# Kernel optimization log

Hardware: AMD Instinct MI355X
Metric: run time of the kernel (lower is better)

## Reference

```python
import jax, jax.numpy as jnp
import numpy as np

B, L, DL, DM, K = 8192, 1, 1024, 1024, 8


def setup_inputs() -> dict:
    key = jax.random.key(0)
    ks = jax.random.split(key, 8)
    s = lambda k, shape, sc=1.0: jax.random.normal(k, shape, jnp.float32) * sc
    return {
        "l_hidden": s(ks[0], (B, L, DL)),
        "m_hidden": s(ks[1], (B, L, DM)),
        "G_l_m": s(ks[2], (DL, K, DM)),   # randn'd each fwd in torch; exposed as input
        "G_m_l": s(ks[3], (DM, K, DL)),
        "l_fc1_w": s(ks[4], (256, DL), 0.02),
        "l_fc1_b": jnp.zeros((256,), jnp.float32),
        "l_fc2_w": s(ks[5], (DL, 256), 0.02),
        "l_fc2_b": jnp.zeros((DL,), jnp.float32),
        "m_fc1_w": s(ks[6], (128, DM), 0.02),
        "m_fc1_b": jnp.zeros((128,), jnp.float32),
        "m_fc2_w": s(ks[7], (DM, 128), 0.02),
        "m_fc2_b": jnp.zeros((DM,), jnp.float32),
    }


def _cross(h_a, h_b, G, g_vec):
    """One direction of the cross-share unit.
    h_a: [B,L,Da], h_b: [B,L,Db], G: [Da,K,Db], g_vec: [B,L,Da]. L must be 1.
    Broadcasts G over batch instead of torch's .repeat (same math, no 256GB copy).
    """
    b, l, da = h_a.shape
    k = G.shape[1]
    # l_hidden @ reshape(G, [Da, K*Db]) -> reshape to [B, L*K, Db]
    s = jnp.einsum('bld,dke->blke', h_a, G).reshape(b, l * k, -1)      # [B,L*K,Db]
    # tanh( shared @ h_b^T ) -> [B, L*K, L]
    t = jnp.tanh(jnp.einsum('bke,bse->bks', s, h_b))                    # [B,L*K,L]
    # reshape [B,L,K,L] -> permute [B,L,L,K] -> [B,L*L,K]
    t = t.reshape(b, l, k, l).transpose(0, 1, 3, 2).reshape(b, l * l, k)
    g = jnp.tile(g_vec, (1, k, 1))                                      # [B,L*K,Da] (L=1 -> [B,K,Da])
    vec = jnp.matmul(t, g)                                              # [B,L*L,Da]
    attn = jax.nn.softmax(vec, axis=-1)
    out = h_a + attn * h_a
    return out, attn


def reference(l_hidden, m_hidden, G_l_m, G_m_l,
              l_fc1_w, l_fc1_b, l_fc2_w, l_fc2_b,
              m_fc1_w, m_fc1_b, m_fc2_w, m_fc2_b):
    # dropout(0.3) is identity in eval mode
    G_vec_l = (l_hidden @ l_fc1_w.T + l_fc1_b) @ l_fc2_w.T + l_fc2_b   # [B,L,DL]
    G_vec_m = (m_hidden @ m_fc1_w.T + m_fc1_b) @ m_fc2_w.T + m_fc2_b   # [B,L,DM]
    l_out, l_attn = _cross(l_hidden, m_hidden, G_l_m, G_vec_l)
    m_out, m_attn = _cross(m_hidden, l_hidden, G_m_l, G_vec_m)
    return l_out, m_out, l_attn, m_attn
```

## Files before the change

kernel.cpp:

```cpp
#include <hip/hip_runtime.h>


#define NB 8192
#define DD 1024

typedef __bf16 bf16x8 __attribute__((ext_vector_type(8)));
typedef float f32x4 __attribute__((ext_vector_type(4)));

__device__ __forceinline__ unsigned short f2bf(float f) {
  unsigned u = __float_as_uint(f);
  u += 0x7FFFu + ((u >> 16) & 1u);
  return (unsigned short)(u >> 16);
}
__device__ __forceinline__ float bf2f(unsigned short h) {
  return __uint_as_float(((unsigned)h) << 16);
}

__global__ __launch_bounds__(256) void split_cast_k(
    const float* __restrict__ in, unsigned short* __restrict__ hi,
    unsigned short* __restrict__ lo, int n4) {
  int i = blockIdx.x * 256 + threadIdx.x;
  if (i >= n4) return;
  float4 v = reinterpret_cast<const float4*>(in)[i];
  float vv[4] = {v.x, v.y, v.z, v.w};
  unsigned short hh[4], ll[4];
#pragma unroll
  for (int c = 0; c < 4; ++c) {
    hh[c] = f2bf(vv[c]);
    ll[c] = f2bf(vv[c] - bf2f(hh[c]));
  }
  reinterpret_cast<ushort4*>(hi)[i] = make_ushort4(hh[0], hh[1], hh[2], hh[3]);
  reinterpret_cast<ushort4*>(lo)[i] = make_ushort4(ll[0], ll[1], ll[2], ll[3]);
}

__global__ __launch_bounds__(256) void transpose_split_k(
    const float* __restrict__ G, unsigned short* __restrict__ bhi,
    unsigned short* __restrict__ blo) {
  __shared__ float t[32][33];
  int c0 = blockIdx.x * 32;
  int d0 = blockIdx.y * 32;
  int tx = threadIdx.x & 31;
  int tg = threadIdx.x >> 5;
#pragma unroll
  for (int s = 0; s < 4; ++s) {
    int dr = tg * 4 + s;
    t[dr][tx] = G[(size_t)(d0 + dr) * 8192 + c0 + tx];
  }
  __syncthreads();
#pragma unroll
  for (int s = 0; s < 4; ++s) {
    int cr = tg * 4 + s;
    float v = t[tx][cr];
    size_t o = (size_t)(c0 + cr) * 1024 + d0 + tx;
    unsigned short h = f2bf(v);
    bhi[o] = h;
    blo[o] = f2bf(v - bf2f(h));
  }
}

__global__ __launch_bounds__(256) void wct_k(
    const float* __restrict__ w1, const float* __restrict__ b1,
    const float* __restrict__ w2, const float* __restrict__ b2, int J,
    unsigned short* __restrict__ bhi, unsigned short* __restrict__ blo,
    float* __restrict__ bc) {
  __shared__ float w2row[256];
  int n = blockIdx.x;
  int tid = threadIdx.x;
  if (tid < J) w2row[tid] = w2[n * J + tid];
  __syncthreads();
#pragma unroll
  for (int s = 0; s < 4; ++s) {
    int i = tid + s * 256;
    float acc = 0.f;
    for (int j = 0; j < J; ++j) acc = fmaf(w2row[j], w1[j * 1024 + i], acc);
    size_t o = (size_t)(8192 + n) * 1024 + i;
    unsigned short h = f2bf(acc);
    bhi[o] = h;
    blo[o] = f2bf(acc - bf2f(h));
  }
  if (tid == 0) {
    float acc = 0.f;
    for (int j = 0; j < J; ++j) acc = fmaf(w2row[j], b1[j], acc);
    bc[n] = acc + b2[n];
  }
}

#define SBAR() do { asm volatile("" ::: "memory"); __builtin_amdgcn_s_barrier(); asm volatile("" ::: "memory"); } while (0)
#define WAITV0() asm volatile("s_waitcnt vmcnt(0)" ::: "memory")
#define WAITV2() asm volatile("s_waitcnt vmcnt(2)" ::: "memory")

#define GLOAD(SRC, DST)                                              \
  __builtin_amdgcn_global_load_lds(                                  \
      (const __attribute__((address_space(1))) void*)(SRC),          \
      (__attribute__((address_space(3))) void*)(lds + (DST)), 16, 0, 0)

__global__ __launch_bounds__(512, 2) void gemm_k(
    const unsigned short* __restrict__ Ahi_, const unsigned short* __restrict__ Alo_,
    const unsigned short* __restrict__ Bhi_, const unsigned short* __restrict__ Blo_,
    const float* __restrict__ hb, float* __restrict__ gvec, float* __restrict__ x) {
  __shared__ __align__(16) char lds[131072];
  const char* Ah = (const char*)Ahi_;
  const char* Al = (const char*)Alo_;
  const char* Bh = (const char*)Bhi_;
  const char* Bl = (const char*)Blo_;

  const int tid = threadIdx.x;
  const int lane = tid & 63;
  const int wid = tid >> 6;
  const int wm = wid >> 2, wn = wid & 3;

  const int bid = blockIdx.x;
  const int xcd = bid & 7;
  const int j = bid >> 3;
  const int by = xcd * 4 + (j & 3);
  const int bx = j >> 2;
  const int m0 = by * 256;
  const int n0 = bx * 256;
  const bool isg = (n0 >= 8192);
  const int nt = isg ? 16 : 48;

  const int rowl = tid >> 3;
  const int colsw = ((tid & 7) ^ ((tid >> 3) & 7)) << 4;
  const int s0 = ((lane >> 4) ^ (lane & 7)) << 4;
  const int s1 = s0 ^ 64;

  f32x4 acc[4][4][2] = {};

  auto stage = [&](int tl, int q) {
    if (tl >= nt) return;
    const int seg = tl >> 4;
    const char* mat;
    int rowbase, dst;
    if (q < 2) {
      mat = (seg == 1) ? Al : Ah;
      rowbase = m0 + q * 128;
      dst = (tl & 1) * 32768 + q * 16384;
    } else {
      mat = (seg == 2) ? Bl : Bh;
      rowbase = n0 + (q - 2) * 128;
      dst = 65536 + (tl & 1) * 32768 + (q - 2) * 16384;
    }
    const char* src = mat + (size_t)(rowbase + rowl) * 2048 + ((tl & 15) << 7) + colsw;
    dst += wid * 1024;
    GLOAD(src, dst);
    GLOAD(src + 64 * 2048, dst + 8192);
  };

  auto ldA = [&](bf16x8 (*d)[2], int qa, int cb) {
    const char* p = lds + cb + qa * 16384 + (wm * 64 + (lane & 15)) * 128;
#pragma unroll
    for (int f = 0; f < 4; ++f) {
      d[f][0] = *reinterpret_cast<const bf16x8*>(p + f * 2048 + s0);
      d[f][1] = *reinterpret_cast<const bf16x8*>(p + f * 2048 + s1);
    }
  };
  auto ldB = [&](bf16x8 (*d)[2], int qb, int cb) {
    const char* p = lds + 65536 + cb + qb * 16384 + (wn * 32 + (lane & 15)) * 128;
#pragma unroll
    for (int g = 0; g < 2; ++g) {
      d[g][0] = *reinterpret_cast<const bf16x8*>(p + g * 2048 + s0);
      d[g][1] = *reinterpret_cast<const bf16x8*>(p + g * 2048 + s1);
    }
  };
  auto mm = [&](f32x4 (*ac)[2], bf16x8 (*aa)[2], bf16x8 (*bb)[2]) {
#pragma unroll
    for (int f = 0; f < 4; ++f)
#pragma unroll
      for (int g = 0; g < 2; ++g) {
        ac[f][g] = __builtin_amdgcn_mfma_f32_16x16x32_bf16(aa[f][0], bb[g][0], ac[f][g], 0, 0, 0);
        ac[f][g] = __builtin_amdgcn_mfma_f32_16x16x32_bf16(aa[f][1], bb[g][1], ac[f][g], 0, 0, 0);
      }
  };

  stage(0, 0); stage(0, 2); stage(0, 3); stage(0, 1);
  WAITV2();
  SBAR();

  bf16x8 af[4][2], af2[4][2], bv[2][2], bv2[2][2];
  for (int t = 0; t < nt; ++t) {
    const int cb = (t & 1) * 32768;
    ldA(af, 0, cb);
    ldB(bv, 0, cb);
    ldB(bv2, 1, cb);
    stage(t + 1, 0);
    __builtin_amdgcn_s_setprio(1);
    mm(acc[0], af, bv);
    __builtin_amdgcn_s_setprio(0);
    if (t + 1 < nt) { WAITV2(); } else { WAITV0(); }
    SBAR();
    ldA(af2, 1, cb);
    stage(t + 1, 2);
    __builtin_amdgcn_s_setprio(1);
    mm(acc[1], af, bv2);
    __builtin_amdgcn_s_setprio(0);
    SBAR();
    stage(t + 1, 3);
    __builtin_amdgcn_s_setprio(1);
    mm(acc[2], af2, bv2);
    __builtin_amdgcn_s_setprio(0);
    SBAR();
    stage(t + 1, 1);
    __builtin_amdgcn_s_setprio(1);
    mm(acc[3], af2, bv);
    __builtin_amdgcn_s_setprio(0);
    WAITV2();
    SBAR();
  }

  const int coll = lane & 15;
  const int rg = (lane >> 4) * 4;
  if (isg) {
#pragma unroll
    for (int q = 0; q < 4; ++q) {
      const int qm = (q >= 2);
      const int qn = (q == 1 || q == 2);
#pragma unroll
      for (int f = 0; f < 4; ++f)
#pragma unroll
        for (int rr = 0; rr < 4; ++rr) {
          const int row = m0 + qm * 128 + wm * 64 + f * 16 + rg + rr;
#pragma unroll
          for (int g = 0; g < 2; ++g) {
            const int gcol = (n0 - 8192) + qn * 128 + wn * 32 + g * 16 + coll;
            gvec[(size_t)row * 1024 + gcol] = acc[q][f][g][rr];
          }
        }
    }
  } else {
    const int kidx = n0 >> 10;
    const int ebase = (n0 & 1023) + wn * 32 + coll;
#pragma unroll
    for (int qm = 0; qm < 2; ++qm) {
      f32x4 (*acA)[2] = acc[qm ? 3 : 0];
      f32x4 (*acB)[2] = acc[qm ? 2 : 1];
#pragma unroll
      for (int f = 0; f < 4; ++f)
#pragma unroll
        for (int rr = 0; rr < 4; ++rr) {
          const int row = m0 + qm * 128 + wm * 64 + f * 16 + rg + rr;
          const float* hr = hb + (size_t)row * 1024 + ebase;
          float tmp = acA[f][0][rr] * hr[0] + acA[f][1][rr] * hr[16] +
                      acB[f][0][rr] * hr[128] + acB[f][1][rr] * hr[144];
#pragma unroll
          for (int s = 1; s < 16; s <<= 1) tmp += __shfl_xor(tmp, s);
          if (coll == 0) atomicAdd(&x[row * 8 + kidx], tmp);
        }
    }
  }
}

__global__ __launch_bounds__(256) void finalize_k(
    const float* __restrict__ xk, const float* __restrict__ gvec,
    const float* __restrict__ bc, const float* __restrict__ ha,
    float* __restrict__ out, float* __restrict__ attn) {
  int b = blockIdx.x;
  int tid = threadIdx.x;
  float S = 0.f;
#pragma unroll
  for (int k = 0; k < 8; ++k) S += tanhf(xk[b * 8 + k]);
  float v[4];
  float mx = -3.4e38f;
#pragma unroll
  for (int s = 0; s < 4; ++s) {
    int d = tid + s * 256;
    v[s] = S * (gvec[(size_t)b * 1024 + d] + bc[d]);
    mx = fmaxf(mx, v[s]);
  }
  __shared__ float red[8];
#pragma unroll
  for (int off = 32; off >= 1; off >>= 1) mx = fmaxf(mx, __shfl_xor(mx, off));
  int lane = tid & 63, w = tid >> 6;
  if (lane == 0) red[w] = mx;
  __syncthreads();
  float m = fmaxf(fmaxf(red[0], red[1]), fmaxf(red[2], red[3]));
  float e[4], sum = 0.f;
#pragma unroll
  for (int s = 0; s < 4; ++s) { e[s] = __expf(v[s] - m); sum += e[s]; }
#pragma unroll
  for (int off = 32; off >= 1; off >>= 1) sum += __shfl_xor(sum, off);
  if (lane == 0) red[4 + w] = sum;
  __syncthreads();
  float inv = 1.f / (red[4] + red[5] + red[6] + red[7]);
#pragma unroll
  for (int s = 0; s < 4; ++s) {
    int d = tid + s * 256;
    float a = e[s] * inv;
    attn[(size_t)b * 1024 + d] = a;
    float h = ha[(size_t)b * 1024 + d];
    out[(size_t)b * 1024 + d] = fmaf(a, h, h);
  }
}

extern "C" void kernel_launch(void* const* d_in, const int* in_sizes, int n_in,
                              void* d_out, int out_size, void* d_ws, size_t ws_size,
                              hipStream_t stream) {
  const float* l_hidden = (const float*)d_in[0];
  const float* m_hidden = (const float*)d_in[1];
  const float* G_l_m = (const float*)d_in[2];
  const float* G_m_l = (const float*)d_in[3];
  const float* l_fc1_w = (const float*)d_in[4];
  const float* l_fc1_b = (const float*)d_in[5];
  const float* l_fc2_w = (const float*)d_in[6];
  const float* l_fc2_b = (const float*)d_in[7];
  const float* m_fc1_w = (const float*)d_in[8];
  const float* m_fc1_b = (const float*)d_in[9];
  const float* m_fc2_w = (const float*)d_in[10];
  const float* m_fc2_b = (const float*)d_in[11];
  float* out = (float*)d_out;

  char* ws = (char*)d_ws;
  unsigned short* Ahi = (unsigned short*)(ws);
  unsigned short* Alo = (unsigned short*)(ws + 16777216);
  unsigned short* Bhi = (unsigned short*)(ws + 33554432);
  unsigned short* Blo = (unsigned short*)(ws + 52428800);
  float* gvec = (float*)(ws + 71303168);
  float* x = (float*)(ws + 104857600);
  float* bc = (float*)(ws + 105381888);

  hipMemsetAsync(x, 0, 2 * NB * 8 * sizeof(float), stream);

  const size_t BD = (size_t)NB * DD;
  dim3 gemmGrid(1152);

  split_cast_k<<<(int)(BD / 4 / 256), 256, 0, stream>>>(l_hidden, Ahi, Alo, (int)(BD / 4));
  transpose_split_k<<<dim3(256, 32), 256, 0, stream>>>(G_l_m, Bhi, Blo);
  wct_k<<<1024, 256, 0, stream>>>(l_fc1_w, l_fc1_b, l_fc2_w, l_fc2_b, 256, Bhi, Blo, bc);
  gemm_k<<<gemmGrid, 512, 0, stream>>>(Ahi, Alo, Bhi, Blo, m_hidden, gvec, x);
  finalize_k<<<NB, 256, 0, stream>>>(x, gvec, bc, l_hidden, out, out + 2 * BD);

  split_cast_k<<<(int)(BD / 4 / 256), 256, 0, stream>>>(m_hidden, Ahi, Alo, (int)(BD / 4));
  transpose_split_k<<<dim3(256, 32), 256, 0, stream>>>(G_m_l, Bhi, Blo);
  wct_k<<<1024, 256, 0, stream>>>(m_fc1_w, m_fc1_b, m_fc2_w, m_fc2_b, 128, Bhi, Blo, bc);
  gemm_k<<<gemmGrid, 512, 0, stream>>>(Ahi, Alo, Bhi, Blo, l_hidden, gvec, x + NB * 8);
  finalize_k<<<NB, 256, 0, stream>>>(x + NB * 8, gvec, bc, m_hidden, out + BD, out + 3 * BD);
}
```

Before: 1.060 ms.

## Deepen GEMM global-to-LDS prefetch pipeline and preload next-tile fragments

Restructures the main GEMM loop so global-to-LDS staging runs further ahead, issuing half of tile t+2 while tile t is computed, and waits on vmcnt(4) instead of vmcnt(2). The A and B fragments for the next tile are loaded into registers during the last MFMA phases of the current tile, so LDS reads overlap compute. Launch bounds drop from 2 to 1 block per CU to free registers for the extra fragment buffer. This lowers occupancy and relies on correct stage/barrier ordering across the double-buffered LDS.

```diff
diff --git a/kernel.cpp b/kernel.cpp
--- a/kernel.cpp
+++ b/kernel.cpp
@@ -87,14 +87,14 @@
 
 #define SBAR() do { asm volatile("" ::: "memory"); __builtin_amdgcn_s_barrier(); asm volatile("" ::: "memory"); } while (0)
 #define WAITV0() asm volatile("s_waitcnt vmcnt(0)" ::: "memory")
-#define WAITV2() asm volatile("s_waitcnt vmcnt(2)" ::: "memory")
+#define WAITV4() asm volatile("s_waitcnt vmcnt(4)" ::: "memory")
 
 #define GLOAD(SRC, DST)                                              \
   __builtin_amdgcn_global_load_lds(                                  \
       (const __attribute__((address_space(1))) void*)(SRC),          \
       (__attribute__((address_space(3))) void*)(lds + (DST)), 16, 0, 0)
 
-__global__ __launch_bounds__(512, 2) void gemm_k(
+__global__ __launch_bounds__(512, 1) void gemm_k(
     const unsigned short* __restrict__ Ahi_, const unsigned short* __restrict__ Alo_,
     const unsigned short* __restrict__ Bhi_, const unsigned short* __restrict__ Blo_,
     const float* __restrict__ hb, float* __restrict__ gvec, float* __restrict__ x) {
@@ -173,38 +173,48 @@
   };
 
   stage(0, 0); stage(0, 2); stage(0, 3); stage(0, 1);
-  WAITV2();
+  stage(1, 0); stage(1, 2);
+  WAITV4();
   SBAR();
 
-  bf16x8 af[4][2], af2[4][2], bv[2][2], bv2[2][2];
+  bf16x8 af[4][2], af2[4][2], bv[2][2], bv2[2][2], bvN[2][2];
+  ldA(af, 0, 0);
+  ldB(bv, 0, 0);
+
   for (int t = 0; t < nt; ++t) {
     const int cb = (t & 1) * 32768;
-    ldA(af, 0, cb);
-    ldB(bv, 0, cb);
+    const int cbN = cb ^ 32768;
     ldB(bv2, 1, cb);
-    stage(t + 1, 0);
+    ldA(af2, 1, cb);
     __builtin_amdgcn_s_setprio(1);
     mm(acc[0], af, bv);
     __builtin_amdgcn_s_setprio(0);
-    if (t + 1 < nt) { WAITV2(); } else { WAITV0(); }
     SBAR();
-    ldA(af2, 1, cb);
-    stage(t + 1, 2);
     __builtin_amdgcn_s_setprio(1);
     mm(acc[1], af, bv2);
     __builtin_amdgcn_s_setprio(0);
+    stage(t + 1, 3); stage(t + 1, 1);
+    if (t + 1 < nt) { WAITV4(); }
     SBAR();
-    stage(t + 1, 3);
+    ldA(af, 0, cbN);
     __builtin_amdgcn_s_setprio(1);
     mm(acc[2], af2, bv2);
     __builtin_amdgcn_s_setprio(0);
     SBAR();
-    stage(t + 1, 1);
+    ldB(bvN, 0, cbN);
     __builtin_amdgcn_s_setprio(1);
     mm(acc[3], af2, bv);
     __builtin_amdgcn_s_setprio(0);
-    WAITV2();
+    stage(t + 2, 0); stage(t + 2, 2);
+    if (t + 1 < nt) {
+      if (t + 2 < nt) { WAITV4(); } else { WAITV0(); }
+    }
     SBAR();
+#pragma unroll
+    for (int g = 0; g < 2; ++g) {
+      bv[g][0] = bvN[g][0];
+      bv[g][1] = bvN[g][1];
+    }
   }
 
   const int coll = lane & 15;
```

New measurement: 1.077 ms. About the same (+1.5%).

## Deepen GEMM pipeline to prefetch two tiles ahead with register double-buffering

Applied to the files above, without the earlier changes.

Restructures the main GEMM loop so global-to-LDS staging runs two k-tiles ahead instead of one, with vmcnt waits relaxed from 2 to 6 outstanding loads. LDS fragments for the next tile are loaded into registers during the current tile's MFMAs. The quadrant order changes, so the epilogue index mapping is updated to match. Launch bounds drop to one block per CU, which frees registers for the extra buffers but halves occupancy and relies on the deeper prefetch to hide latency.

```diff
diff --git a/kernel.cpp b/kernel.cpp
--- a/kernel.cpp
+++ b/kernel.cpp
@@ -87,14 +87,14 @@
 
 #define SBAR() do { asm volatile("" ::: "memory"); __builtin_amdgcn_s_barrier(); asm volatile("" ::: "memory"); } while (0)
 #define WAITV0() asm volatile("s_waitcnt vmcnt(0)" ::: "memory")
-#define WAITV2() asm volatile("s_waitcnt vmcnt(2)" ::: "memory")
+#define WAITV6() asm volatile("s_waitcnt vmcnt(6)" ::: "memory")
 
 #define GLOAD(SRC, DST)                                              \
   __builtin_amdgcn_global_load_lds(                                  \
       (const __attribute__((address_space(1))) void*)(SRC),          \
       (__attribute__((address_space(3))) void*)(lds + (DST)), 16, 0, 0)
 
-__global__ __launch_bounds__(512, 2) void gemm_k(
+__global__ __launch_bounds__(512, 1) void gemm_k(
     const unsigned short* __restrict__ Ahi_, const unsigned short* __restrict__ Alo_,
     const unsigned short* __restrict__ Bhi_, const unsigned short* __restrict__ Blo_,
     const float* __restrict__ hb, float* __restrict__ gvec, float* __restrict__ x) {
@@ -172,38 +172,49 @@
       }
   };
 
-  stage(0, 0); stage(0, 2); stage(0, 3); stage(0, 1);
-  WAITV2();
+  stage(0, 0); stage(0, 2);
+  stage(0, 3); stage(0, 1); stage(1, 0); stage(1, 2);
+  WAITV6();
   SBAR();
-
-  bf16x8 af[4][2], af2[4][2], bv[2][2], bv2[2][2];
+  bf16x8 rA0[4][2], rA1[4][2], rB0[2][2], rB1[2][2];
+  ldA(rA0, 0, 0);
+  ldB(rB0, 0, 0);
+
   for (int t = 0; t < nt; ++t) {
     const int cb = (t & 1) * 32768;
-    ldA(af, 0, cb);
-    ldB(bv, 0, cb);
-    ldB(bv2, 1, cb);
-    stage(t + 1, 0);
+    const int cbN = cb ^ 32768;
+    const bool tail = (t + 2 >= nt);
+    ldB(rB1, 1, cb);
+    stage(t + 1, 3);
+    if (tail) { WAITV0(); } else { WAITV6(); }
+    SBAR();
     __builtin_amdgcn_s_setprio(1);
-    mm(acc[0], af, bv);
+    mm(acc[0], rA0, rB0);
     __builtin_amdgcn_s_setprio(0);
-    if (t + 1 < nt) { WAITV2(); } else { WAITV0(); }
-    SBAR();
-    ldA(af2, 1, cb);
-    stage(t + 1, 2);
+    SBAR();
+    ldA(rA1, 1, cb);
+    stage(t + 1, 1);
+    if (tail) { WAITV0(); } else { WAITV6(); }
+    SBAR();
     __builtin_amdgcn_s_setprio(1);
-    mm(acc[1], af, bv2);
+    mm(acc[1], rA0, rB1);
     __builtin_amdgcn_s_setprio(0);
     SBAR();
-    stage(t + 1, 3);
+    if (t + 1 < nt) ldA(rA0, 0, cbN);
+    stage(t + 2, 0);
+    if (tail) { WAITV0(); } else { WAITV6(); }
+    SBAR();
     __builtin_amdgcn_s_setprio(1);
-    mm(acc[2], af2, bv2);
+    mm(acc[2], rA1, rB0);
     __builtin_amdgcn_s_setprio(0);
     SBAR();
-    stage(t + 1, 1);
+    if (t + 1 < nt) ldB(rB0, 0, cbN);
+    stage(t + 2, 2);
+    if (tail) { WAITV0(); } else { WAITV6(); }
+    SBAR();
     __builtin_amdgcn_s_setprio(1);
-    mm(acc[3], af2, bv);
+    mm(acc[3], rA1, rB1);
     __builtin_amdgcn_s_setprio(0);
-    WAITV2();
     SBAR();
   }
 
@@ -212,8 +223,8 @@
   if (isg) {
 #pragma unroll
     for (int q = 0; q < 4; ++q) {
-      const int qm = (q >= 2);
-      const int qn = (q == 1 || q == 2);
+      const int qm = q >> 1;
+      const int qn = q & 1;
 #pragma unroll
       for (int f = 0; f < 4; ++f)
 #pragma unroll
@@ -231,8 +242,8 @@
     const int ebase = (n0 & 1023) + wn * 32 + coll;
 #pragma unroll
     for (int qm = 0; qm < 2; ++qm) {
-      f32x4 (*acA)[2] = acc[qm ? 3 : 0];
-      f32x4 (*acB)[2] = acc[qm ? 2 : 1];
+      f32x4 (*acA)[2] = acc[qm ? 2 : 0];
+      f32x4 (*acB)[2] = acc[qm ? 3 : 1];
 #pragma unroll
       for (int f = 0; f < 4; ++f)
 #pragma unroll
```

After: 1.097 ms. 1.03x slower.

## Load B operand directly from global into registers, halve LDS, remap tile grid

Applied to the files above, without the earlier changes.

The B-operand tiles now go straight from global memory into registers, and only A is staged through LDS. This halves shared memory to 64KB and drops the B LDS round-trip and its bank traffic. The pipeline is reordered around new vmcnt waits, launch bounds drop to one block per CU, and the block-to-XCD mapping changes to a different tile swizzle. The risks are uncoalesced and exposed global latency on the direct B loads, extra barriers, and lower occupancy.

```diff
diff --git a/kernel.cpp b/kernel.cpp
--- a/kernel.cpp
+++ b/kernel.cpp
@@ -86,19 +86,19 @@
 }
 
 #define SBAR() do { asm volatile("" ::: "memory"); __builtin_amdgcn_s_barrier(); asm volatile("" ::: "memory"); } while (0)
-#define WAITV0() asm volatile("s_waitcnt vmcnt(0)" ::: "memory")
-#define WAITV2() asm volatile("s_waitcnt vmcnt(2)" ::: "memory")
+#define WAITV6() asm volatile("s_waitcnt vmcnt(6)" ::: "memory")
+#define WAITV8() asm volatile("s_waitcnt vmcnt(8)" ::: "memory")
 
 #define GLOAD(SRC, DST)                                              \
   __builtin_amdgcn_global_load_lds(                                  \
       (const __attribute__((address_space(1))) void*)(SRC),          \
       (__attribute__((address_space(3))) void*)(lds + (DST)), 16, 0, 0)
 
-__global__ __launch_bounds__(512, 2) void gemm_k(
+__global__ __launch_bounds__(512, 1) void gemm_k(
     const unsigned short* __restrict__ Ahi_, const unsigned short* __restrict__ Alo_,
     const unsigned short* __restrict__ Bhi_, const unsigned short* __restrict__ Blo_,
     const float* __restrict__ hb, float* __restrict__ gvec, float* __restrict__ x) {
-  __shared__ __align__(16) char lds[131072];
+  __shared__ __align__(16) char lds[65536];
   const char* Ah = (const char*)Ahi_;
   const char* Al = (const char*)Alo_;
   const char* Bh = (const char*)Bhi_;
@@ -112,8 +112,8 @@
   const int bid = blockIdx.x;
   const int xcd = bid & 7;
   const int j = bid >> 3;
-  const int by = xcd * 4 + (j & 3);
-  const int bx = j >> 2;
+  const int by = (xcd >> 1) * 8 + (j & 7);
+  const int bx = ((j >> 3) << 1) + (xcd & 1);
   const int m0 = by * 256;
   const int n0 = bx * 256;
   const bool isg = (n0 >= 8192);
@@ -124,24 +124,21 @@
   const int s0 = ((lane >> 4) ^ (lane & 7)) << 4;
   const int s1 = s0 ^ 64;
 
+  const char* pB[2][2];
+#pragma unroll
+  for (int qb = 0; qb < 2; ++qb)
+#pragma unroll
+    for (int g = 0; g < 2; ++g)
+      pB[qb][g] = Bh + (size_t)(n0 + qb * 128 + wn * 32 + g * 16 + (lane & 15)) * 2048 +
+                  (lane >> 4) * 16;
+  const long long dBlo = Bl - Bh;
+
   f32x4 acc[4][4][2] = {};
 
-  auto stage = [&](int tl, int q) {
-    if (tl >= nt) return;
-    const int seg = tl >> 4;
-    const char* mat;
-    int rowbase, dst;
-    if (q < 2) {
-      mat = (seg == 1) ? Al : Ah;
-      rowbase = m0 + q * 128;
-      dst = (tl & 1) * 32768 + q * 16384;
-    } else {
-      mat = (seg == 2) ? Bl : Bh;
-      rowbase = n0 + (q - 2) * 128;
-      dst = 65536 + (tl & 1) * 32768 + (q - 2) * 16384;
-    }
-    const char* src = mat + (size_t)(rowbase + rowl) * 2048 + ((tl & 15) << 7) + colsw;
-    dst += wid * 1024;
+  auto stageA = [&](int tl, int par, int q) {
+    const char* mat = ((tl >> 4) == 1) ? Al : Ah;
+    const char* src = mat + (size_t)(m0 + q * 128 + rowl) * 2048 + ((tl & 15) << 7) + colsw;
+    const int dst = par * 32768 + q * 16384 + wid * 1024;
     GLOAD(src, dst);
     GLOAD(src + 64 * 2048, dst + 8192);
   };
@@ -154,12 +151,14 @@
       d[f][1] = *reinterpret_cast<const bf16x8*>(p + f * 2048 + s1);
     }
   };
-  auto ldB = [&](bf16x8 (*d)[2], int qb, int cb) {
-    const char* p = lds + 65536 + cb + qb * 16384 + (wn * 32 + (lane & 15)) * 128;
+  auto ldBdir = [&](bf16x8 (*d)[2], int qb, int tl) {
+    const long long segoff = ((tl >> 4) == 2) ? dBlo : 0;
+    const int kb = (tl & 15) << 7;
 #pragma unroll
     for (int g = 0; g < 2; ++g) {
-      d[g][0] = *reinterpret_cast<const bf16x8*>(p + g * 2048 + s0);
-      d[g][1] = *reinterpret_cast<const bf16x8*>(p + g * 2048 + s1);
+      const char* p = pB[qb][g] + segoff + kb;
+      d[g][0] = *reinterpret_cast<const bf16x8*>(p);
+      d[g][1] = *reinterpret_cast<const bf16x8*>(p + 64);
     }
   };
   auto mm = [&](f32x4 (*ac)[2], bf16x8 (*aa)[2], bf16x8 (*bb)[2]) {
@@ -172,38 +171,47 @@
       }
   };
 
-  stage(0, 0); stage(0, 2); stage(0, 3); stage(0, 1);
-  WAITV2();
+  bf16x8 af[4][2], af2[4][2], bv[2][2], bv2[2][2];
+
+  stageA(0, 0, 0); stageA(0, 0, 1);
+  ldBdir(bv, 0, 0);
+  ldBdir(bv2, 1, 0);
+  WAITV8();
   SBAR();
-
-  bf16x8 af[4][2], af2[4][2], bv[2][2], bv2[2][2];
+  ldA(af, 0, 0);
+
   for (int t = 0; t < nt; ++t) {
     const int cb = (t & 1) * 32768;
-    ldA(af, 0, cb);
-    ldB(bv, 0, cb);
-    ldB(bv2, 1, cb);
-    stage(t + 1, 0);
+    const int cbN = cb ^ 32768;
+    const int parN = (t + 1) & 1;
+    const int tn = (t + 1 < nt) ? (t + 1) : (nt - 1);
+    ldA(af2, 1, cb);
+    stageA(tn, parN, 0);
+    SBAR();
     __builtin_amdgcn_s_setprio(1);
     mm(acc[0], af, bv);
     __builtin_amdgcn_s_setprio(0);
-    if (t + 1 < nt) { WAITV2(); } else { WAITV0(); }
-    SBAR();
-    ldA(af2, 1, cb);
-    stage(t + 1, 2);
+    SBAR();
+    stageA(tn, parN, 1);
+    SBAR();
     __builtin_amdgcn_s_setprio(1);
-    mm(acc[1], af, bv2);
+    mm(acc[1], af2, bv);
     __builtin_amdgcn_s_setprio(0);
     SBAR();
-    stage(t + 1, 3);
+    ldBdir(bv, 0, tn);
+    SBAR();
     __builtin_amdgcn_s_setprio(1);
-    mm(acc[2], af2, bv2);
+    mm(acc[2], af, bv2);
     __builtin_amdgcn_s_setprio(0);
     SBAR();
-    stage(t + 1, 1);
+    WAITV6();
+    SBAR();
+    ldA(af, 0, cbN);
     __builtin_amdgcn_s_setprio(1);
-    mm(acc[3], af2, bv);
+    mm(acc[3], af2, bv2);
     __builtin_amdgcn_s_setprio(0);
-    WAITV2();
+    ldBdir(bv2, 1, tn);
+    WAITV8();
     SBAR();
   }
 
@@ -212,8 +220,8 @@
   if (isg) {
 #pragma unroll
     for (int q = 0; q < 4; ++q) {
-      const int qm = (q >= 2);
-      const int qn = (q == 1 || q == 2);
+      const int qm = q & 1;
+      const int qn = q >> 1;
 #pragma unroll
       for (int f = 0; f < 4; ++f)
 #pragma unroll
@@ -231,8 +239,8 @@
     const int ebase = (n0 & 1023) + wn * 32 + coll;
 #pragma unroll
     for (int qm = 0; qm < 2; ++qm) {
-      f32x4 (*acA)[2] = acc[qm ? 3 : 0];
-      f32x4 (*acB)[2] = acc[qm ? 2 : 1];
+      f32x4 (*acA)[2] = acc[qm ? 1 : 0];
+      f32x4 (*acB)[2] = acc[qm ? 3 : 2];
 #pragma unroll
       for (int f = 0; f < 4; ++f)
 #pragma unroll
```

After: 1.497 ms. +41.1%, slower.
